# Performance work log

Measured on AMD Instinct MI355X. Metric: run time of the kernel, lower is better.

## Reference

```python
import jax, jax.numpy as jnp
import numpy as np

B, N, M, C, H, G, KD = 4, 1024, 128, 512, 8, 3, 16
DH = C // H


def setup_inputs() -> dict:
    key = jax.random.key(0)
    ks = jax.random.split(key, 12)
    def w(k, shape, fan_in):
        return jax.random.normal(k, shape, jnp.float32) / np.sqrt(fan_in)
    return {
        'pairwise_g': jax.random.normal(ks[0], (B, N, N, G), jnp.float32),
        'coset_functions': jax.random.normal(ks[1], (B, N, C), jnp.float32),
        'mask': jnp.ones((B, N), dtype=bool),
        'W1': w(ks[2], (G, KD), G), 'b1': jnp.zeros((KD,), jnp.float32),
        'W2': w(ks[3], (KD, KD), KD), 'b2': jnp.zeros((KD,), jnp.float32),
        'W3': w(ks[4], (KD, H), KD), 'b3': jnp.zeros((H,), jnp.float32),
        'Wq': w(ks[5], (C, C), C), 'bq': jnp.zeros((C,), jnp.float32),
        'Wk': w(ks[6], (C, C), C), 'bk': jnp.zeros((C,), jnp.float32),
        'Wv': w(ks[7], (C, C), C), 'bv': jnp.zeros((C,), jnp.float32),
        'Wo': w(ks[8], (C, C), C), 'bo': jnp.zeros((C,), jnp.float32),
    }


def _gather_nbhd(x, idx):
    # x: (B, N, ...) gathered along point axis with idx: (B, Nq, M) -> (B, Nq, M, ...)
    return jax.vmap(lambda a, i: a[i])(x, idx)


def reference(pairwise_g, coset_functions, mask,
              W1, b1, W2, b2, W3, b3,
              Wq, bq, Wk, bk, Wv, bv, Wo, bo):
    swish = jax.nn.silu
    # --- neighborhood extraction: topk smallest group distance (mc_samples path) ---
    dists = jnp.linalg.norm(pairwise_g, axis=-1)                  # (B,N,N)
    dists = jnp.where(mask[:, None, :], dists, jnp.float32(1e8))
    _, nbhd_idx = jax.lax.top_k(-dists, M)                        # (B,N,M) nearest M

    nbhd_g = jnp.take_along_axis(pairwise_g, nbhd_idx[..., None], axis=2)  # (B,N,M,G)
    nbhd_mask = _gather_nbhd(mask, nbhd_idx)                      # (B,N,M)

    # --- location kernel: per-pair MLP on lie-algebra offsets -> per-head logits ---
    h = swish(nbhd_g @ W1 + b1)
    h = swish(h @ W2 + b2)
    loc = h @ W3 + b3                                             # (B,N,M,H)

    # --- feature kernel: multi-head dot product, keys gathered at neighborhoods ---
    q = (coset_functions @ Wq + bq).reshape(B, N, H, DH)
    k = coset_functions @ Wk + bk                                 # (B,N,C)
    k_n = _gather_nbhd(k, nbhd_idx).reshape(B, N, M, H, DH)
    dot = jnp.einsum('bnhd,bnmhd->bnmh', q, k_n) / jnp.sqrt(jnp.float32(DH))

    # --- masked softmax over neighborhood axis ---
    pre = loc + dot
    pre = jnp.where(nbhd_mask[..., None], pre, jnp.float32(-1e38))
    attn = jax.nn.softmax(pre, axis=2)                            # (B,N,M,H)

    # --- value projection, gather, weighted aggregate, output projection ---
    v = coset_functions @ Wv + bv                                 # (B,N,C)
    v_n = _gather_nbhd(v, nbhd_idx).reshape(B, N, M, H, DH)
    out = jnp.einsum('bnmh,bnmhd->bnhd', attn, v_n).reshape(B, N, C)
    out = out @ Wo + bo                                           # (B,N,C)
    return out
```

## Files before the change

kernel.cpp:

```cpp
#include <hip/hip_runtime.h>
#include <hip/hip_bf16.h>
#include <math.h>

#define NB 4
#define NPTS 1024
#define MN 128
#define CH 512
#define NH 8
#define DHD 64
#define NG 3
#define KDIM 16

typedef unsigned short u16;
typedef unsigned short u16x8 __attribute__((ext_vector_type(8)));
typedef short short8 __attribute__((ext_vector_type(8)));
typedef float f32x4 __attribute__((ext_vector_type(4)));

#define FEXP(x) __expf(x)

__device__ __forceinline__ float b2f(u16 u) {
  return __uint_as_float(((unsigned)u) << 16);
}
__device__ __forceinline__ u16 f2b(float f) {
  unsigned x = __float_as_uint(f);
  return (u16)((x + 0x7FFFu + ((x >> 16) & 1u)) >> 16);
}

__global__ __launch_bounds__(256) void cvt_bf16(const float* __restrict__ x,
                                                u16* __restrict__ y) {
  int i = blockIdx.x * 256 + threadIdx.x;
  float4 a = ((const float4*)x)[i * 2];
  float4 b = ((const float4*)x)[i * 2 + 1];
  ushort4 o0, o1;
  o0.x = f2b(a.x); o0.y = f2b(a.y); o0.z = f2b(a.z); o0.w = f2b(a.w);
  o1.x = f2b(b.x); o1.y = f2b(b.y); o1.z = f2b(b.z); o1.w = f2b(b.w);
  ((ushort4*)y)[i * 2] = o0;
  ((ushort4*)y)[i * 2 + 1] = o1;
}

__global__ __launch_bounds__(256) void transpose_cvt(
    const float* __restrict__ W0, const float* __restrict__ W1,
    const float* __restrict__ W2, const float* __restrict__ W3,
    u16* __restrict__ T0, u16* __restrict__ T1, u16* __restrict__ T2,
    u16* __restrict__ T3) {
  const float* src; u16* dst;
  if (blockIdx.z == 0)      { src = W0; dst = T0; }
  else if (blockIdx.z == 1) { src = W1; dst = T1; }
  else if (blockIdx.z == 2) { src = W2; dst = T2; }
  else                      { src = W3; dst = T3; }
  __shared__ float tile[32][33];
  const int k0 = blockIdx.y * 32, n0 = blockIdx.x * 32;
  const int r8 = threadIdx.x >> 5, c = threadIdx.x & 31;
#pragma unroll
  for (int i = 0; i < 4; i++)
    tile[r8 + i * 8][c] = src[(size_t)(k0 + r8 + i * 8) * CH + n0 + c];
  __syncthreads();
#pragma unroll
  for (int i = 0; i < 4; i++)
    dst[(size_t)(n0 + r8 + i * 8) * CH + k0 + c] = f2b(tile[c][r8 + i * 8]);
}

__device__ __forceinline__ void gstore(float* p, float v) { *p = v; }
__device__ __forceinline__ void gstore(u16* p, float v) { *p = f2b(v); }

template <typename OT>
__global__ __launch_bounds__(256) void mfma_gemm3(
    const u16* __restrict__ A,
    const u16* __restrict__ Wa, const float* __restrict__ ba,
    const u16* __restrict__ Wb, const float* __restrict__ bb_,
    const u16* __restrict__ Wc, const float* __restrict__ bc,
    OT* __restrict__ Ya, OT* __restrict__ Yb, OT* __restrict__ Yc) {
  const u16* W; const float* bias; OT* Y;
  if (blockIdx.z == 0)      { W = Wa; bias = ba;  Y = Ya; }
  else if (blockIdx.z == 1) { W = Wb; bias = bb_; Y = Yb; }
  else                      { W = Wc; bias = bc;  Y = Yc; }

  __shared__ u16 As[128][40];
  __shared__ u16 Bs[128][40];

  const int t = threadIdx.x;
  const int row0 = blockIdx.y * 128;
  const int col0 = blockIdx.x * 128;
  const int r2 = t >> 1;
  const int sb = (t & 1) * 16;
  const int w = t >> 6, lane = t & 63;
  const int q4 = lane >> 4, l16 = lane & 15;
  const int wr = (w & 1) * 64, wc = (w >> 1) * 64;

  f32x4 acc[4][4];
#pragma unroll
  for (int mt = 0; mt < 4; mt++)
#pragma unroll
    for (int nt = 0; nt < 4; nt++) acc[mt][nt] = (f32x4){0.f, 0.f, 0.f, 0.f};

  for (int kt = 0; kt < CH; kt += 32) {
    u16x8 av0 = *(const u16x8*)(A + (size_t)(row0 + r2) * CH + kt + sb);
    u16x8 av1 = *(const u16x8*)(A + (size_t)(row0 + r2) * CH + kt + sb + 8);
    u16x8 bv0 = *(const u16x8*)(W + (size_t)(col0 + r2) * CH + kt + sb);
    u16x8 bv1 = *(const u16x8*)(W + (size_t)(col0 + r2) * CH + kt + sb + 8);
    *(u16x8*)&As[r2][sb] = av0;
    *(u16x8*)&As[r2][sb + 8] = av1;
    *(u16x8*)&Bs[r2][sb] = bv0;
    *(u16x8*)&Bs[r2][sb + 8] = bv1;
    __syncthreads();
    short8 af[4], bf[4];
#pragma unroll
    for (int mt = 0; mt < 4; mt++)
      af[mt] = *(const short8*)&As[wr + mt * 16 + l16][q4 * 8];
#pragma unroll
    for (int nt = 0; nt < 4; nt++)
      bf[nt] = *(const short8*)&Bs[wc + nt * 16 + l16][q4 * 8];
#pragma unroll
    for (int mt = 0; mt < 4; mt++)
#pragma unroll
      for (int nt = 0; nt < 4; nt++)
        acc[mt][nt] = __builtin_amdgcn_mfma_f32_16x16x32_bf16(
            af[mt], bf[nt], acc[mt][nt], 0, 0, 0);
    __syncthreads();
  }

#pragma unroll
  for (int nt = 0; nt < 4; nt++) {
    const int col = col0 + wc + nt * 16 + l16;
    const float bb = bias[col];
#pragma unroll
    for (int mt = 0; mt < 4; mt++) {
#pragma unroll
      for (int r = 0; r < 4; r++) {
        const int row = row0 + wr + mt * 16 + q4 * 4 + r;
        gstore(Y + (size_t)row * CH + col, acc[mt][nt][r] + bb);
      }
    }
  }
}

__global__ __launch_bounds__(256) void select_loc(
    const float* __restrict__ g, int* __restrict__ idx_out,
    const float* __restrict__ W1, const float* __restrict__ b1,
    const float* __restrict__ W2, const float* __restrict__ b2,
    const float* __restrict__ W3, const float* __restrict__ b3,
    u16* __restrict__ locw) {
  const int bn = blockIdx.x;
  const int t = threadIdx.x;
  const int wv = t >> 6, lane = t & 63;
  __shared__ unsigned int key[NPTS];
  __shared__ int hist[4][256];
  __shared__ int incl[256];
  __shared__ int wtot[4];
  __shared__ int selidx[MN];
  __shared__ unsigned int s_prefix;
  __shared__ unsigned int s_selmask;
  __shared__ int s_target, s_done, s_cless, s_ctie, s_fill;

  const float* row = g + (size_t)bn * (NPTS * NG);
#pragma unroll
  for (int r = 0; r < 4; r++) {
    int j = t + 256 * r;
    float g0 = row[j * 3 + 0];
    float g1 = row[j * 3 + 1];
    float g2 = row[j * 3 + 2];
    float ss = __fadd_rn(__fadd_rn(__fmul_rn(g0, g0), __fmul_rn(g1, g1)),
                         __fmul_rn(g2, g2));
    key[j] = __float_as_uint(__fsqrt_rn(ss));
  }
  if (t == 0) {
    s_prefix = 0u; s_target = MN - 1; s_done = 0;
    s_selmask = 0xFFFFFFFFu;
  }
  __syncthreads();

  for (int pass = 3; pass >= 0; pass--) {
    if (s_done) break;
    const unsigned int pref = s_prefix;
    const int target = s_target;
    const int sh = 8 * pass;
    const unsigned int himask = (pass == 3) ? 0u : (0xFFFFFFFFu << (sh + 8));
#pragma unroll
    for (int w = 0; w < 4; w++) hist[w][t] = 0;
    __syncthreads();
#pragma unroll
    for (int r = 0; r < 4; r++) {
      unsigned int kk = key[t + 256 * r];
      if ((kk & himask) == (pref & himask))
        atomicAdd(&hist[wv][(kk >> sh) & 255], 1);
    }
    __syncthreads();
    int sv = hist[0][t] + hist[1][t] + hist[2][t] + hist[3][t];
#pragma unroll
    for (int o = 1; o < 64; o <<= 1) {
      int n = __shfl_up(sv, o);
      if (lane >= o) sv += n;
    }
    if (lane == 63) wtot[wv] = sv;
    __syncthreads();
    int base = 0;
#pragma unroll
    for (int w = 0; w < 4; w++) base += (w < wv) ? wtot[w] : 0;
    sv += base;
    incl[t] = sv;
    __syncthreads();
    int below = (t == 0) ? 0 : incl[t - 1];
    int mine = incl[t];
    __syncthreads();
    if (mine > target && below <= target) {
      s_prefix = pref | ((unsigned int)t << sh);
      s_target = target - below;
      if (mine - below == target - below + 1) {
        s_done = 1;
        s_selmask = 0xFFFFFFFFu << sh;
      }
    }
    __syncthreads();
  }

  const unsigned int sm = s_selmask;
  const unsigned int T = s_prefix;
  const int need = s_target + 1;
  if (t == 0) { s_cless = 0; s_ctie = 0; s_fill = 0; }
  __syncthreads();
  int* orow = idx_out + bn * MN;
#pragma unroll
  for (int r = 0; r < 4; r++) {
    int j = t + 256 * r;
    unsigned int kk = key[j] & sm;
    if (kk < T) {
      int p = atomicAdd(&s_cless, 1);
      if (p < MN) { orow[p] = j; selidx[p] = j; }
    } else if (kk == T) {
      atomicAdd(&s_ctie, 1);
    }
  }
  __syncthreads();
  const int L = s_cless;
  const int ctie = s_ctie;
  __syncthreads();
  if (ctie == need) {
    for (int r = 0; r < 4; r++) {
      int j = t + 256 * r;
      if ((key[j] & sm) == T) {
        int p = atomicAdd(&s_fill, 1);
        int q = L + p;
        if (q < MN) { orow[q] = j; selidx[q] = j; }
      }
    }
  } else {
    for (int r = 0; r < 4; r++) {
      int j = t + 256 * r;
      if ((key[j] & sm) == T) {
        int rank = 0;
        for (int jj = 0; jj < j; jj++) rank += ((key[jj] & sm) == T) ? 1 : 0;
        int q = L + rank;
        if (rank < need && q >= 0 && q < MN) { orow[q] = j; selidx[q] = j; }
      }
    }
  }
  __syncthreads();

  if (t < MN) {
    const int j = selidx[t] & (NPTS - 1);
    const float* gp = g + ((size_t)bn * NPTS + j) * NG;
    float g0 = gp[0], g1 = gp[1], g2 = gp[2];
    float h1[KDIM], h2[KDIM];
#pragma unroll
    for (int u = 0; u < KDIM; u++) {
      float s = W1[u] * g0 + W1[KDIM + u] * g1 + W1[2 * KDIM + u] * g2 + b1[u];
      h1[u] = s / (1.f + FEXP(-s));
    }
#pragma unroll
    for (int vv = 0; vv < KDIM; vv++) {
      float s = b2[vv];
#pragma unroll
      for (int u = 0; u < KDIM; u++) s += h1[u] * W2[u * KDIM + vv];
      h2[vv] = s / (1.f + FEXP(-s));
    }
    u16* op = locw + ((size_t)bn * MN + t) * NH;
#pragma unroll
    for (int h = 0; h < NH; h++) {
      float s = b3[h];
#pragma unroll
      for (int vv = 0; vv < KDIM; vv++) s += h2[vv] * W3[vv * NH + h];
      op[h] = f2b(s);
    }
  }
}

#define WPB 4

__global__ __launch_bounds__(256) void attn_kernel(
    const u16* __restrict__ qg, const u16* __restrict__ kg,
    const u16* __restrict__ vg, const u16* __restrict__ locw,
    const int* __restrict__ idxg, u16* __restrict__ outg) {
  const int t = threadIdx.x;
  const int wv = t >> 6;
  const int lane = t & 63;
  const int bn = blockIdx.x * WPB + wv;
  const int b = bn >> 10;

  __shared__ int nidx[WPB][MN];
  nidx[wv][lane] = idxg[bn * MN + lane] & (NPTS - 1);
  nidx[wv][lane + 64] = idxg[bn * MN + 64 + lane] & (NPTS - 1);
  __syncthreads();

  u16x8 qv = *(const u16x8*)(qg + (size_t)bn * CH + lane * 8);
  float q[8];
#pragma unroll
  for (int e = 0; e < 8; e++) q[e] = b2f(qv[e]);
  const int hl = lane >> 3;
  const u16* kb = kg + (size_t)b * NPTS * CH;
  const u16* vb = vg + (size_t)b * NPTS * CH;
  const u16* lb = locw + (size_t)bn * MN * NH;

  float M = -INFINITY, L = 0.f;
  float a[8];
#pragma unroll
  for (int e = 0; e < 8; e++) a[e] = 0.f;

  for (int m = 0; m < MN; m += 2) {
    const int j0 = nidx[wv][m];
    const int j1 = nidx[wv][m + 1];
    u16x8 k0v = *(const u16x8*)(kb + (size_t)j0 * CH + lane * 8);
    u16x8 k1v = *(const u16x8*)(kb + (size_t)j1 * CH + lane * 8);
    u16x8 v0v = *(const u16x8*)(vb + (size_t)j0 * CH + lane * 8);
    u16x8 v1v = *(const u16x8*)(vb + (size_t)j1 * CH + lane * 8);
    float l0 = b2f(lb[m * NH + hl]);
    float l1 = b2f(lb[(m + 1) * NH + hl]);

    float p0 = 0.f, p1 = 0.f;
#pragma unroll
    for (int e = 0; e < 8; e++) {
      p0 += q[e] * b2f(k0v[e]);
      p1 += q[e] * b2f(k1v[e]);
    }
    p0 += __shfl_xor(p0, 1); p0 += __shfl_xor(p0, 2); p0 += __shfl_xor(p0, 4);
    p1 += __shfl_xor(p1, 1); p1 += __shfl_xor(p1, 2); p1 += __shfl_xor(p1, 4);
    p0 = p0 * 0.125f + l0;
    p1 = p1 * 0.125f + l1;

    float mx = fmaxf(M, fmaxf(p0, p1));
    float alpha = FEXP(M - mx);
    float e0 = FEXP(p0 - mx);
    float e1 = FEXP(p1 - mx);
    L = L * alpha + e0 + e1;
#pragma unroll
    for (int e = 0; e < 8; e++)
      a[e] = a[e] * alpha + e0 * b2f(v0v[e]) + e1 * b2f(v1v[e]);
    M = mx;
  }

  const float inv = 1.f / L;
  u16x8 o;
#pragma unroll
  for (int e = 0; e < 8; e++) o[e] = f2b(a[e] * inv);
  *(u16x8*)(outg + (size_t)bn * CH + lane * 8) = o;
}

extern "C" void kernel_launch(void* const* d_in, const int* in_sizes, int n_in,
                              void* d_out, int out_size, void* d_ws, size_t ws_size,
                              hipStream_t stream) {
  (void)in_sizes; (void)n_in; (void)out_size; (void)ws_size;
  const float* pg = (const float*)d_in[0];
  const float* cf = (const float*)d_in[1];
  const float* W1 = (const float*)d_in[3];
  const float* b1 = (const float*)d_in[4];
  const float* W2 = (const float*)d_in[5];
  const float* b2 = (const float*)d_in[6];
  const float* W3 = (const float*)d_in[7];
  const float* b3 = (const float*)d_in[8];
  const float* Wq = (const float*)d_in[9];
  const float* bq = (const float*)d_in[10];
  const float* Wk = (const float*)d_in[11];
  const float* bk = (const float*)d_in[12];
  const float* Wv = (const float*)d_in[13];
  const float* bv = (const float*)d_in[14];
  const float* Wo = (const float*)d_in[15];
  const float* bo = (const float*)d_in[16];
  float* out = (float*)d_out;

  char* p = (char*)d_ws;
  u16* cfb = (u16*)p;
  u16* WTq = (u16*)(p + (4 << 20));
  u16* WTk = WTq + 262144;
  u16* WTv = WTk + 262144;
  u16* WTo = WTv + 262144;
  u16* qw = (u16*)(p + (6 << 20));
  u16* kw = (u16*)(p + (10 << 20));
  u16* vw = (u16*)(p + (14 << 20));
  int* idxw = (int*)(p + (18 << 20));
  u16* locw = (u16*)(p + (20 << 20));
  u16* awb = qw;

  const int R = NB * NPTS;

  cvt_bf16<<<dim3(R * CH / 8 / 256), 256, 0, stream>>>(cf, cfb);
  transpose_cvt<<<dim3(16, 16, 4), 256, 0, stream>>>(Wq, Wk, Wv, Wo, WTq, WTk,
                                                     WTv, WTo);
  mfma_gemm3<u16><<<dim3(CH / 128, R / 128, 3), 256, 0, stream>>>(
      cfb, WTq, bq, WTk, bk, WTv, bv, qw, kw, vw);
  select_loc<<<dim3(R), 256, 0, stream>>>(pg, idxw, W1, b1, W2, b2, W3, b3,
                                          locw);
  attn_kernel<<<dim3(R / WPB), 256, 0, stream>>>(qw, kw, vw, locw, idxw, awb);
  mfma_gemm3<float><<<dim3(CH / 128, R / 128, 1), 256, 0, stream>>>(
      awb, WTo, bo, WTo, bo, WTo, bo, out, out, out);
}
```

Measured before the change: 248.7 us.

## Split attention neighborhood across two waves and use bf16 dot2 intrinsics

Each query point is now handled by two wavefronts, each taking half of the 128 neighbors with its own online softmax. The partial max, sum and accumulators are merged through shared memory at the end. The QK dot product uses the bf16 fdot2 builtin when the compiler provides it, and value accumulation uses packed float2 math. This doubles the number of waves in flight to hide gather latency, at the cost of an extra barrier, a shared-memory merge, and a launch bound that caps registers.

```diff
diff --git a/kernel.cpp b/kernel.cpp
--- a/kernel.cpp
+++ b/kernel.cpp
@@ -15,8 +15,16 @@
 typedef unsigned short u16x8 __attribute__((ext_vector_type(8)));
 typedef short short8 __attribute__((ext_vector_type(8)));
 typedef float f32x4 __attribute__((ext_vector_type(4)));
+typedef float f32x2 __attribute__((ext_vector_type(2)));
 
 #define FEXP(x) __expf(x)
+
+#if defined(__has_builtin)
+#if __has_builtin(__builtin_amdgcn_fdot2_f32_bf16)
+#define HAS_DOT2 1
+typedef __bf16 bf16x2 __attribute__((ext_vector_type(2)));
+#endif
+#endif
 
 __device__ __forceinline__ float b2f(u16 u) {
   return __uint_as_float(((unsigned)u) << 16);
@@ -24,6 +32,12 @@
 __device__ __forceinline__ u16 f2b(float f) {
   unsigned x = __float_as_uint(f);
   return (u16)((x + 0x7FFFu + ((x >> 16) & 1u)) >> 16);
+}
+__device__ __forceinline__ f32x2 bpair(unsigned u) {
+  f32x2 r;
+  r.x = __uint_as_float(u << 16);
+  r.y = __uint_as_float(u & 0xFFFF0000u);
+  return r;
 }
 
 __global__ __launch_bounds__(256) void cvt_bf16(const float* __restrict__ x,
@@ -284,53 +298,81 @@
   }
 }
 
-#define WPB 4
-
-__global__ __launch_bounds__(256) void attn_kernel(
+__global__ __launch_bounds__(256, 8) void attn_kernel(
     const u16* __restrict__ qg, const u16* __restrict__ kg,
     const u16* __restrict__ vg, const u16* __restrict__ locw,
     const int* __restrict__ idxg, u16* __restrict__ outg) {
   const int t = threadIdx.x;
   const int wv = t >> 6;
   const int lane = t & 63;
-  const int bn = blockIdx.x * WPB + wv;
+  const int pt = wv >> 1;
+  const int half = wv & 1;
+  const int bn = blockIdx.x * 2 + pt;
   const int b = bn >> 10;
 
-  __shared__ int nidx[WPB][MN];
-  nidx[wv][lane] = idxg[bn * MN + lane] & (NPTS - 1);
-  nidx[wv][lane + 64] = idxg[bn * MN + 64 + lane] & (NPTS - 1);
+  __shared__ int nidx[2][MN];
+  __shared__ float red[2][64][11];
+
+  nidx[pt][half * 64 + lane] = idxg[bn * MN + half * 64 + lane] & (NPTS - 1);
   __syncthreads();
 
   u16x8 qv = *(const u16x8*)(qg + (size_t)bn * CH + lane * 8);
-  float q[8];
-#pragma unroll
-  for (int e = 0; e < 8; e++) q[e] = b2f(qv[e]);
   const int hl = lane >> 3;
   const u16* kb = kg + (size_t)b * NPTS * CH;
   const u16* vb = vg + (size_t)b * NPTS * CH;
-  const u16* lb = locw + (size_t)bn * MN * NH;
+  const u16* lb = locw + (size_t)bn * MN * NH + hl;
 
   float M = -INFINITY, L = 0.f;
-  float a[8];
-#pragma unroll
-  for (int e = 0; e < 8; e++) a[e] = 0.f;
-
-  for (int m = 0; m < MN; m += 2) {
-    const int j0 = nidx[wv][m];
-    const int j1 = nidx[wv][m + 1];
+  f32x2 acc[4];
+#pragma unroll
+  for (int i = 0; i < 4; i++) acc[i] = (f32x2){0.f, 0.f};
+
+#if defined(HAS_DOT2)
+  bf16x2 qh[4];
+  {
+    union { u16x8 v; unsigned u[4]; } uq; uq.v = qv;
+#pragma unroll
+    for (int i = 0; i < 4; i++) qh[i] = __builtin_bit_cast(bf16x2, uq.u[i]);
+  }
+#else
+  float qf[8];
+#pragma unroll
+  for (int e = 0; e < 8; e++) qf[e] = b2f(qv[e]);
+#endif
+
+  const int mb = half * 64;
+  const int* nrow = &nidx[pt][mb];
+  for (int mi = 0; mi < 64; mi += 2) {
+    const int j0 = nrow[mi];
+    const int j1 = nrow[mi + 1];
     u16x8 k0v = *(const u16x8*)(kb + (size_t)j0 * CH + lane * 8);
     u16x8 k1v = *(const u16x8*)(kb + (size_t)j1 * CH + lane * 8);
     u16x8 v0v = *(const u16x8*)(vb + (size_t)j0 * CH + lane * 8);
     u16x8 v1v = *(const u16x8*)(vb + (size_t)j1 * CH + lane * 8);
-    float l0 = b2f(lb[m * NH + hl]);
-    float l1 = b2f(lb[(m + 1) * NH + hl]);
+    float l0 = b2f(lb[(mb + mi) * NH]);
+    float l1 = b2f(lb[(mb + mi + 1) * NH]);
+
+    union { u16x8 v; unsigned u[4]; } uk0, uk1, uv0, uv1;
+    uk0.v = k0v; uk1.v = k1v; uv0.v = v0v; uv1.v = v1v;
 
     float p0 = 0.f, p1 = 0.f;
-#pragma unroll
-    for (int e = 0; e < 8; e++) {
-      p0 += q[e] * b2f(k0v[e]);
-      p1 += q[e] * b2f(k1v[e]);
-    }
+#if defined(HAS_DOT2)
+#pragma unroll
+    for (int e = 0; e < 4; e++) {
+      p0 = __builtin_amdgcn_fdot2_f32_bf16(
+          qh[e], __builtin_bit_cast(bf16x2, uk0.u[e]), p0, false);
+      p1 = __builtin_amdgcn_fdot2_f32_bf16(
+          qh[e], __builtin_bit_cast(bf16x2, uk1.u[e]), p1, false);
+    }
+#else
+#pragma unroll
+    for (int e = 0; e < 4; e++) {
+      f32x2 kp0 = bpair(uk0.u[e]);
+      f32x2 kp1 = bpair(uk1.u[e]);
+      p0 += qf[2 * e] * kp0.x + qf[2 * e + 1] * kp0.y;
+      p1 += qf[2 * e] * kp1.x + qf[2 * e + 1] * kp1.y;
+    }
+#endif
     p0 += __shfl_xor(p0, 1); p0 += __shfl_xor(p0, 2); p0 += __shfl_xor(p0, 4);
     p1 += __shfl_xor(p1, 1); p1 += __shfl_xor(p1, 2); p1 += __shfl_xor(p1, 4);
     p0 = p0 * 0.125f + l0;
@@ -341,17 +383,41 @@
     float e0 = FEXP(p0 - mx);
     float e1 = FEXP(p1 - mx);
     L = L * alpha + e0 + e1;
-#pragma unroll
-    for (int e = 0; e < 8; e++)
-      a[e] = a[e] * alpha + e0 * b2f(v0v[e]) + e1 * b2f(v1v[e]);
+    const f32x2 av = (f32x2){alpha, alpha};
+    const f32x2 e0v = (f32x2){e0, e0};
+    const f32x2 e1v = (f32x2){e1, e1};
+#pragma unroll
+    for (int i = 0; i < 4; i++)
+      acc[i] = acc[i] * av + bpair(uv0.u[i]) * e0v + bpair(uv1.u[i]) * e1v;
     M = mx;
   }
 
-  const float inv = 1.f / L;
-  u16x8 o;
-#pragma unroll
-  for (int e = 0; e < 8; e++) o[e] = f2b(a[e] * inv);
-  *(u16x8*)(outg + (size_t)bn * CH + lane * 8) = o;
+  if (half) {
+    float* rp = &red[pt][lane][0];
+#pragma unroll
+    for (int i = 0; i < 4; i++) {
+      rp[2 * i] = acc[i].x;
+      rp[2 * i + 1] = acc[i].y;
+    }
+    rp[8] = M;
+    rp[9] = L;
+  }
+  __syncthreads();
+  if (!half) {
+    const float* rp = &red[pt][lane][0];
+    const float M1 = rp[8], L1 = rp[9];
+    const float mx = fmaxf(M, M1);
+    const float s0 = FEXP(M - mx);
+    const float s1 = FEXP(M1 - mx);
+    const float inv = 1.f / (L * s0 + L1 * s1);
+    u16x8 o;
+#pragma unroll
+    for (int i = 0; i < 4; i++) {
+      o[2 * i] = f2b((acc[i].x * s0 + rp[2 * i] * s1) * inv);
+      o[2 * i + 1] = f2b((acc[i].y * s0 + rp[2 * i + 1] * s1) * inv);
+    }
+    *(u16x8*)(outg + (size_t)bn * CH + lane * 8) = o;
+  }
 }
 
 extern "C" void kernel_launch(void* const* d_in, const int* in_sizes, int n_in,
@@ -398,7 +464,7 @@
       cfb, WTq, bq, WTk, bk, WTv, bv, qw, kw, vw);
   select_loc<<<dim3(R), 256, 0, stream>>>(pg, idxw, W1, b1, W2, b2, W3, b3,
                                           locw);
-  attn_kernel<<<dim3(R / WPB), 256, 0, stream>>>(qw, kw, vw, locw, idxw, awb);
+  attn_kernel<<<dim3(R / 2), 256, 0, stream>>>(qw, kw, vw, locw, idxw, awb);
   mfma_gemm3<float><<<dim3(CH / 128, R / 128, 1), 256, 0, stream>>>(
       awb, WTo, bo, WTo, bo, WTo, bo, out, out, out);
 }
```

Measured after the change: 233.3 us. 6.2% less time.
